# Kernel optimization log

Hardware: AMD Instinct MI355X
Metric: run time of the kernel (lower is better)

The kernel has to match this reference:

```python
import jax, jax.numpy as jnp
import numpy as np

T, H, E, K = 16384, 2880, 128, 4

def setup_inputs() -> dict:
    key = jax.random.key(0)
    k1, k2, k3 = jax.random.split(key, 3)
    return {
        "hidden_states": jax.random.normal(k1, (T, H), dtype=jnp.float32),
        "weight": jax.random.normal(k2, (E, H), dtype=jnp.float32) * 0.02,
        "bias": jax.random.normal(k3, (E,), dtype=jnp.float32) * 0.02,
    }

def reference(hidden_states, weight, bias):
    x = hidden_states.reshape(-1, weight.shape[1])            # [T, H]
    logits = jnp.einsum('th,eh->te', x, weight) + bias        # [T, E]
    top_val, top_idx = jax.lax.top_k(logits, K)               # sorted desc, [T, K]
    top_val = jax.nn.softmax(top_val, axis=-1)
    rows = jnp.arange(logits.shape[0])[:, None]
    scores = jnp.zeros_like(logits).at[rows, top_idx].set(top_val)
    return scores, top_idx
```

## Files before the change

### kernel.cpp

```cpp
#include <hip/hip_runtime.h>
#include <math.h>


#define T_TOK 16384
#define HDIM  2880
#define EEXP  128
#define KTOP  4

#define TM   32
#define NT   256
#define KC   64
#define NCH  (HDIM / KC)
#define XBUF 4096
#define TAU  4e-3f

typedef __attribute__((ext_vector_type(8))) _Float16 f16x8;
typedef __attribute__((ext_vector_type(4))) float    f32x4;

#define MFMA(a, b, c) __builtin_amdgcn_mfma_f32_16x16x32_f16((a), (b), (c), 0, 0, 0)

__global__ __launch_bounds__(256) void w_cvt(
    const float* __restrict__ w, char* __restrict__ wp)
{
    const int gid  = blockIdx.x * 256 + threadIdx.x;
    const int lane = gid & 63;
    const int q    = gid >> 6;
    const int ks   = q & 1;
    const int q2   = q >> 1;
    const int c    = q2 % NCH;
    const int F    = q2 / NCH;
    const int e    = F * 16 + (lane & 15);
    const int k0   = c * 64 + ks * 32 + (lane >> 4) * 8;

    const float* src = w + (size_t)e * HDIM + k0;
    float4 v0 = *(const float4*)(src);
    float4 v1 = *(const float4*)(src + 4);
    union { _Float16 h[8]; uint4 u; } H;
    H.h[0] = (_Float16)v0.x; H.h[1] = (_Float16)v0.y;
    H.h[2] = (_Float16)v0.z; H.h[3] = (_Float16)v0.w;
    H.h[4] = (_Float16)v1.x; H.h[5] = (_Float16)v1.y;
    H.h[6] = (_Float16)v1.z; H.h[7] = (_Float16)v1.w;
    const int tile = (F * NCH + c) * 2 + ks;
    *(uint4*)(wp + (size_t)tile * 1024 + lane * 16) = H.u;
}

static __device__ __forceinline__ void cvt_write128(char* base, int off, float4 v) {
    union { _Float16 h[4]; uint2 u; } U;
    U.h[0] = (_Float16)v.x; U.h[1] = (_Float16)v.y;
    U.h[2] = (_Float16)v.z; U.h[3] = (_Float16)v.w;
    *(uint2*)(base + off) = U.u;
}

__global__ __launch_bounds__(NT, 2) void router_fused(
    const float* __restrict__ x, const char* __restrict__ wp,
    const float* __restrict__ w, const float* __restrict__ bias,
    float* __restrict__ out)
{
    __shared__ char smem[20480];
    const int tid  = threadIdx.x;
    const int tok0 = blockIdx.x * TM;
    const int lane = tid & 63;
    const int wv   = tid >> 6;
    const int r    = lane & 15;
    const int g    = lane >> 4;

    char* xb0 = smem;
    char* xb1 = smem + XBUF;
    char* xb2 = smem + 2 * XBUF;

    int xoff[2];
    const float* xptr[2];
#pragma unroll
    for (int i = 0; i < 2; ++i) {
        int f = tid + i * NT;
        int row = f >> 4, c4 = f & 15;
        xoff[i] = row * 128 + ((((c4 >> 1) ^ (row & 7)) << 4) | ((c4 & 1) << 3));
        xptr[i] = x + (size_t)(tok0 + row) * HDIM + c4 * 4;
    }

    int aoff[2][2];
#pragma unroll
    for (int tf = 0; tf < 2; ++tf) {
        int row = tf * 16 + r;
#pragma unroll
        for (int ks = 0; ks < 2; ++ks)
            aoff[tf][ks] = row * 128 + (((ks * 4 + g) ^ (row & 7)) << 4);
    }

    f32x4 a00 = {0.f, 0.f, 0.f, 0.f}, a01 = a00, a10 = a00, a11 = a00;

#define LOADX(pf, cc) do {                                            \
        pf[0] = *(const float4*)(xptr[0] + (cc) * KC);                \
        pf[1] = *(const float4*)(xptr[1] + (cc) * KC); } while (0)

#define WRITEX(pf, bb) do {                                           \
        cvt_write128((bb), xoff[0], pf[0]);                           \
        cvt_write128((bb), xoff[1], pf[1]); } while (0)

#define LOADW(W, cc) do {                                             \
        _Pragma("unroll")                                             \
        for (int F2 = 0; F2 < 2; ++F2)                                \
        _Pragma("unroll")                                             \
        for (int ks_ = 0; ks_ < 2; ++ks_)                             \
            W[F2*2 + ks_] = *(const f16x8*)(wp +                      \
                (size_t)(((wv*2 + F2) * NCH + (cc)) * 2 + ks_) * 1024 \
                + lane * 16); } while (0)

#define MFMA_CHUNK(cb, W) do {                                        \
        _Pragma("unroll")                                             \
        for (int ks_ = 0; ks_ < 2; ++ks_) {                           \
            f16x8 a0 = *(const f16x8*)((cb) + aoff[0][ks_]);          \
            f16x8 a1 = *(const f16x8*)((cb) + aoff[1][ks_]);          \
            a00 = MFMA(a0, W[ks_],     a00);                          \
            a01 = MFMA(a0, W[2 + ks_], a01);                          \
            a10 = MFMA(a1, W[ks_],     a10);                          \
            a11 = MFMA(a1, W[2 + ks_], a11);                          \
        } } while (0)

    float4 pfA[2], pfB[2], pfC[2];
    f16x8 wA[4], wB[4], wC[4];

    LOADX(pfA, 0); LOADX(pfB, 1); LOADX(pfC, 2);
    LOADW(wA, 0); LOADW(wB, 1);
    WRITEX(pfA, xb0);
    __syncthreads();

    for (int c = 0; c < NCH; c += 3) {
        if (c + 3 < NCH) LOADX(pfA, c + 3);
        LOADW(wC, c + 2);
        MFMA_CHUNK(xb0, wA);
        WRITEX(pfB, xb1);
        __syncthreads();
        if (c + 3 < NCH) LOADW(wA, c + 3);
        if (c + 4 < NCH) LOADX(pfB, c + 4);
        MFMA_CHUNK(xb1, wB);
        WRITEX(pfC, xb2);
        __syncthreads();
        if (c + 4 < NCH) LOADW(wB, c + 4);
        if (c + 5 < NCH) LOADX(pfC, c + 5);
        MFMA_CHUNK(xb2, wC);
        if (c + 3 < NCH) WRITEX(pfA, xb0);
        __syncthreads();
    }

    float* logitsL = (float*)smem;
    const float bv0 = bias[wv * 32 + r];
    const float bv1 = bias[wv * 32 + 16 + r];
#pragma unroll
    for (int q = 0; q < 4; ++q) {
        int m0 = g * 4 + q, m1 = m0 + 16;
        int e0 = wv * 32 + r, e1 = e0 + 16;
        logitsL[m0 * 130 + e0] = a00[q] + bv0;
        logitsL[m0 * 130 + e1] = a01[q] + bv1;
        logitsL[m1 * 130 + e0] = a10[q] + bv0;
        logitsL[m1 * 130 + e1] = a11[q] + bv1;
    }
    float*  cvf = (float*) (smem + 16640);
    int*    cie = (int*)   (smem + 17664);
    int*    flg = (int*)   (smem + 18688);
    double* svd = (double*)(smem + 18816);
    int*    sid = (int*)   (smem + 19840);
    double* cvd = (double*)(smem + 20352);
    __syncthreads();

    {
        const int t = tid >> 3, s = tid & 7;
        float v[8]; int id[8];
#pragma unroll
        for (int k = 0; k < 8; ++k) { v[k] = -3.4e38f; id[k] = 0x7fffffff; }
        for (int jj = 0; jj < 16; ++jj) {
            float lv = logitsL[t * 130 + s * 16 + jj];
            int   e  = s * 16 + jj;
            bool gt[8];
#pragma unroll
            for (int k = 0; k < 8; ++k)
                gt[k] = (lv > v[k]) || (lv == v[k] && e < id[k]);
#pragma unroll
            for (int k = 7; k >= 1; --k)
                if (gt[k - 1]) { v[k] = v[k - 1]; id[k] = id[k - 1]; }
#pragma unroll
            for (int k = 0; k < 8; ++k) {
                bool put = gt[k] && (k == 0 || !gt[k - 1]);
                if (put) { v[k] = lv; id[k] = e; }
            }
        }
#pragma unroll
        for (int rd = 0; rd < 8; ++rd) {
            float hv = v[0]; int hi = id[0];
#pragma unroll
            for (int off = 1; off < 8; off <<= 1) {
                float ov = __shfl_xor(hv, off);
                int   oi = __shfl_xor(hi, off);
                if (ov > hv || (ov == hv && oi < hi)) { hv = ov; hi = oi; }
            }
            if (s == 0) { cvf[t * 8 + rd] = hv; cie[t * 8 + rd] = hi; }
            bool mine = (v[0] == hv) && (id[0] == hi);
            if (mine) {
#pragma unroll
                for (int k = 0; k < 7; ++k) { v[k] = v[k + 1]; id[k] = id[k + 1]; }
                v[7] = -3.4e38f; id[7] = 0x7fffffff;
            }
        }
    }
    __syncthreads();

    if (tid < TM) {
        float gmin = 3.4e38f;
#pragma unroll
        for (int k = 0; k < 4; ++k)
            gmin = fminf(gmin, cvf[tid * 8 + k] - cvf[tid * 8 + k + 1]);
        flg[tid] = (gmin < TAU);
    }
    if (tid < 128) {
        int t2 = tid >> 2, k = tid & 3;
        svd[t2 * 4 + k] = (double)cvf[t2 * 8 + k];
        sid[t2 * 4 + k] = cie[t2 * 8 + k];
    }
    __syncthreads();

    for (int ts = 0; ts < TM; ++ts) {
        if (!flg[ts]) continue;
#pragma unroll
        for (int h2 = 0; h2 < 2; ++h2) {
            const int cand = wv * 2 + h2;
            const int ce = cie[ts * 8 + cand];
            const float4* xr = (const float4*)(x + (size_t)(tok0 + ts) * HDIM);
            const float4* wr = (const float4*)(w + (size_t)ce * HDIM);
            double q0 = 0.0, q1 = 0.0, q2 = 0.0, q3 = 0.0;
            for (int i2 = 0; i2 < 12; ++i2) {
                int fi = lane + i2 * 64;
                if (fi < HDIM / 4) {
                    float4 xv = xr[fi];
                    float4 wv4 = wr[fi];
                    q0 = fma((double)xv.x, (double)wv4.x, q0);
                    q1 = fma((double)xv.y, (double)wv4.y, q1);
                    q2 = fma((double)xv.z, (double)wv4.z, q2);
                    q3 = fma((double)xv.w, (double)wv4.w, q3);
                }
            }
            double accd = (q0 + q2) + (q1 + q3);
#pragma unroll
            for (int off = 32; off > 0; off >>= 1)
                accd += __shfl_xor(accd, off);
            if (lane == 0) cvd[cand] = accd + (double)bias[ce];
        }
        __syncthreads();
        if (tid < 8) {
            double mv = cvd[tid]; int mi2 = cie[ts * 8 + tid];
            int rk = 0;
#pragma unroll
            for (int j2 = 0; j2 < 8; ++j2) {
                double oj = cvd[j2];
                rk += (oj > mv) || (oj == mv && cie[ts * 8 + j2] < mi2);
            }
            if (rk < 4) { svd[ts * 4 + rk] = mv; sid[ts * 4 + rk] = mi2; }
        }
        __syncthreads();
    }

    float* srow = (float*)smem;
    float4 z4 = make_float4(0.f, 0.f, 0.f, 0.f);
#pragma unroll
    for (int i = 0; i < 4; ++i)
        ((float4*)srow)[tid + i * NT] = z4;
    __syncthreads();

    if (tid < TM) {
        double m  = svd[tid * 4];
        double e0 = exp(svd[tid * 4 + 0] - m), e1 = exp(svd[tid * 4 + 1] - m);
        double e2 = exp(svd[tid * 4 + 2] - m), e3 = exp(svd[tid * 4 + 3] - m);
        double inv = 1.0 / ((e0 + e1) + (e2 + e3));
        float* oidx = out + (size_t)T_TOK * EEXP + (size_t)(tok0 + tid) * KTOP;
        int i0 = sid[tid * 4 + 0], i1 = sid[tid * 4 + 1];
        int i2 = sid[tid * 4 + 2], i3 = sid[tid * 4 + 3];
        oidx[0] = (float)i0; oidx[1] = (float)i1;
        oidx[2] = (float)i2; oidx[3] = (float)i3;
        srow[tid * EEXP + i0] = (float)(e0 * inv);
        srow[tid * EEXP + i1] = (float)(e1 * inv);
        srow[tid * EEXP + i2] = (float)(e2 * inv);
        srow[tid * EEXP + i3] = (float)(e3 * inv);
    }
    __syncthreads();

    float4* orow = (float4*)(out + (size_t)tok0 * EEXP);
#pragma unroll
    for (int i = 0; i < 4; ++i)
        orow[tid + i * NT] = ((float4*)srow)[tid + i * NT];
}

extern "C" void kernel_launch(void* const* d_in, const int* in_sizes, int n_in,
                              void* d_out, int out_size, void* d_ws, size_t ws_size,
                              hipStream_t stream) {
    const float* x    = (const float*)d_in[0];
    const float* w    = (const float*)d_in[1];
    const float* bias = (const float*)d_in[2];
    float* out        = (float*)d_out;
    char*  wp         = (char*)d_ws;

    hipLaunchKernelGGL(w_cvt, dim3(180), dim3(256), 0, stream, w, wp);
    hipLaunchKernelGGL(router_fused, dim3(T_TOK / TM), dim3(NT), 0, stream,
                       x, wp, w, bias, out);
}
```

Baseline: 79.23 us.

## Halve token tile to 16 rows per block for higher occupancy

Reduces the token tile per block from 32 to 16, halving shared memory and accumulators and raising the launch-bounds occupancy hint from 2 to 4 blocks per CU. Each wave now does one token-row MFMA set per chunk, which doubles the grid to 1024 blocks. The smem offsets and the top-k and softmax thread ranges are rescaled to match. The cost is that each W tile is reused across half as many tokens, so global and L2 reads of the fp16 weights roughly double.

Measured after the change: 84.28 us. 1.06x slower.

```diff
diff --git a/kernel.cpp b/kernel.cpp
--- a/kernel.cpp
+++ b/kernel.cpp
@@ -7,11 +7,11 @@
 #define EEXP  128
 #define KTOP  4
 
-#define TM   32
+#define TM   16
 #define NT   256
 #define KC   64
 #define NCH  (HDIM / KC)
-#define XBUF 4096
+#define XBUF 2048
 #define TAU  4e-3f
 
 typedef __attribute__((ext_vector_type(8))) _Float16 f16x8;
@@ -51,12 +51,12 @@
     *(uint2*)(base + off) = U.u;
 }
 
-__global__ __launch_bounds__(NT, 2) void router_fused(
+__global__ __launch_bounds__(NT, 4) void router_fused(
     const float* __restrict__ x, const char* __restrict__ wp,
     const float* __restrict__ w, const float* __restrict__ bias,
     float* __restrict__ out)
 {
-    __shared__ char smem[20480];
+    __shared__ char smem[10240];
     const int tid  = threadIdx.x;
     const int tok0 = blockIdx.x * TM;
     const int lane = tid & 63;
@@ -68,34 +68,26 @@
     char* xb1 = smem + XBUF;
     char* xb2 = smem + 2 * XBUF;
 
-    int xoff[2];
-    const float* xptr[2];
-#pragma unroll
-    for (int i = 0; i < 2; ++i) {
-        int f = tid + i * NT;
-        int row = f >> 4, c4 = f & 15;
-        xoff[i] = row * 128 + ((((c4 >> 1) ^ (row & 7)) << 4) | ((c4 & 1) << 3));
-        xptr[i] = x + (size_t)(tok0 + row) * HDIM + c4 * 4;
-    }
-
-    int aoff[2][2];
-#pragma unroll
-    for (int tf = 0; tf < 2; ++tf) {
-        int row = tf * 16 + r;
+    int xoff;
+    const float* xptr;
+    {
+        int row = tid >> 4, c4 = tid & 15;
+        xoff = row * 128 + ((((c4 >> 1) ^ (row & 7)) << 4) | ((c4 & 1) << 3));
+        xptr = x + (size_t)(tok0 + row) * HDIM + c4 * 4;
+    }
+
+    int aoff[2];
+    {
+        int row = r;
 #pragma unroll
         for (int ks = 0; ks < 2; ++ks)
-            aoff[tf][ks] = row * 128 + (((ks * 4 + g) ^ (row & 7)) << 4);
-    }
-
-    f32x4 a00 = {0.f, 0.f, 0.f, 0.f}, a01 = a00, a10 = a00, a11 = a00;
-
-#define LOADX(pf, cc) do {                                            \
-        pf[0] = *(const float4*)(xptr[0] + (cc) * KC);                \
-        pf[1] = *(const float4*)(xptr[1] + (cc) * KC); } while (0)
-
-#define WRITEX(pf, bb) do {                                           \
-        cvt_write128((bb), xoff[0], pf[0]);                           \
-        cvt_write128((bb), xoff[1], pf[1]); } while (0)
+            aoff[ks] = row * 128 + (((ks * 4 + g) ^ (row & 7)) << 4);
+    }
+
+    f32x4 a00 = {0.f, 0.f, 0.f, 0.f}, a01 = a00;
+
+#define LOADX(pf, cc) do { pf = *(const float4*)(xptr + (cc) * KC); } while (0)
+#define WRITEX(pf, bb) do { cvt_write128((bb), xoff, pf); } while (0)
 
 #define LOADW(W, cc) do {                                             \
         _Pragma("unroll")                                             \
@@ -109,15 +101,12 @@
 #define MFMA_CHUNK(cb, W) do {                                        \
         _Pragma("unroll")                                             \
         for (int ks_ = 0; ks_ < 2; ++ks_) {                           \
-            f16x8 a0 = *(const f16x8*)((cb) + aoff[0][ks_]);          \
-            f16x8 a1 = *(const f16x8*)((cb) + aoff[1][ks_]);          \
+            f16x8 a0 = *(const f16x8*)((cb) + aoff[ks_]);             \
             a00 = MFMA(a0, W[ks_],     a00);                          \
             a01 = MFMA(a0, W[2 + ks_], a01);                          \
-            a10 = MFMA(a1, W[ks_],     a10);                          \
-            a11 = MFMA(a1, W[2 + ks_], a11);                          \
         } } while (0)
 
-    float4 pfA[2], pfB[2], pfC[2];
+    float4 pfA, pfB, pfC;
     f16x8 wA[4], wB[4], wC[4];
 
     LOADX(pfA, 0); LOADX(pfB, 1); LOADX(pfC, 2);
@@ -144,26 +133,26 @@
     }
 
     float* logitsL = (float*)smem;
-    const float bv0 = bias[wv * 32 + r];
-    const float bv1 = bias[wv * 32 + 16 + r];
-#pragma unroll
-    for (int q = 0; q < 4; ++q) {
-        int m0 = g * 4 + q, m1 = m0 + 16;
-        int e0 = wv * 32 + r, e1 = e0 + 16;
-        logitsL[m0 * 130 + e0] = a00[q] + bv0;
-        logitsL[m0 * 130 + e1] = a01[q] + bv1;
-        logitsL[m1 * 130 + e0] = a10[q] + bv0;
-        logitsL[m1 * 130 + e1] = a11[q] + bv1;
-    }
-    float*  cvf = (float*) (smem + 16640);
-    int*    cie = (int*)   (smem + 17664);
-    int*    flg = (int*)   (smem + 18688);
-    double* svd = (double*)(smem + 18816);
-    int*    sid = (int*)   (smem + 19840);
-    double* cvd = (double*)(smem + 20352);
-    __syncthreads();
-
     {
+        const float bv0 = bias[wv * 32 + r];
+        const float bv1 = bias[wv * 32 + 16 + r];
+#pragma unroll
+        for (int q = 0; q < 4; ++q) {
+            int tok = g * 4 + q;
+            int e0 = wv * 32 + r, e1 = e0 + 16;
+            logitsL[tok * 130 + e0] = a00[q] + bv0;
+            logitsL[tok * 130 + e1] = a01[q] + bv1;
+        }
+    }
+    float*  cvf = (float*) (smem + 8320);
+    int*    cie = (int*)   (smem + 8832);
+    int*    flg = (int*)   (smem + 9344);
+    double* svd = (double*)(smem + 9408);
+    int*    sid = (int*)   (smem + 9920);
+    double* cvd = (double*)(smem + 10176);
+    __syncthreads();
+
+    if (tid < 128) {
         const int t = tid >> 3, s = tid & 7;
         float v[8]; int id[8];
 #pragma unroll
@@ -211,7 +200,7 @@
             gmin = fminf(gmin, cvf[tid * 8 + k] - cvf[tid * 8 + k + 1]);
         flg[tid] = (gmin < TAU);
     }
-    if (tid < 128) {
+    if (tid < 64) {
         int t2 = tid >> 2, k = tid & 3;
         svd[t2 * 4 + k] = (double)cvf[t2 * 8 + k];
         sid[t2 * 4 + k] = cie[t2 * 8 + k];
@@ -261,7 +250,7 @@
     float* srow = (float*)smem;
     float4 z4 = make_float4(0.f, 0.f, 0.f, 0.f);
 #pragma unroll
-    for (int i = 0; i < 4; ++i)
+    for (int i = 0; i < 2; ++i)
         ((float4*)srow)[tid + i * NT] = z4;
     __syncthreads();
 
@@ -284,7 +273,7 @@
 
     float4* orow = (float4*)(out + (size_t)tok0 * EEXP);
 #pragma unroll
-    for (int i = 0; i < 4; ++i)
+    for (int i = 0; i < 2; ++i)
         orow[tid + i * NT] = ((float4*)srow)[tid + i * NT];
 }
 
```
